# Kernel tuning notes

Hardware: AMD Instinct MI355X
Metric: run time of the kernel (lower is better)

Reference implementation:

```python
import jax, jax.numpy as jnp
import numpy as np

H = 51  # hidden size hard-coded in the module


def setup_inputs() -> dict:
    key = jax.random.key(0)
    ks = jax.random.split(key, 11)
    B, T = 1024, 512
    s = 1.0 / np.sqrt(H)
    u = lambda k, shape: jax.random.uniform(k, shape, jnp.float32, -s, s)
    return {
        "input": jax.random.normal(ks[0], (B, T), jnp.float32),
        "Wih1": u(ks[1], (4 * H, 1)),
        "Whh1": u(ks[2], (4 * H, H)),
        "bih1": u(ks[3], (4 * H,)),
        "bhh1": u(ks[4], (4 * H,)),
        "Wih2": u(ks[5], (4 * H, H)),
        "Whh2": u(ks[6], (4 * H, H)),
        "bih2": u(ks[7], (4 * H,)),
        "bhh2": u(ks[8], (4 * H,)),
        "Wl": u(ks[9], (1, H)),
        "bl": u(ks[10], (1,)),
        "future": 64,
    }


def _lstm_cell(x, h, c, Wih, Whh, b):
    # x: [B, in], h/c: [B, H]; PyTorch LSTMCell gate order: i, f, g, o
    g = x @ Wih.T + h @ Whh.T + b  # [B, 4H]
    i, f, gg, o = jnp.split(g, 4, axis=-1)
    c = jax.nn.sigmoid(f) * c + jax.nn.sigmoid(i) * jnp.tanh(gg)
    h = jax.nn.sigmoid(o) * jnp.tanh(c)
    return h, c


def reference(input, Wih1, Whh1, bih1, bhh1, Wih2, Whh2, bih2, bhh2, Wl, bl, future):
    B = input.shape[0]
    b1 = bih1 + bhh1
    b2 = bih2 + bhh2
    z = jnp.zeros((B, H), input.dtype)

    def step(carry, x_t):
        h1, c1, h2, c2 = carry
        h1, c1 = _lstm_cell(x_t[:, None], h1, c1, Wih1, Whh1, b1)
        h2, c2 = _lstm_cell(h1, h2, c2, Wih2, Whh2, b2)
        out = h2 @ Wl.T + bl  # [B, 1]
        return (h1, c1, h2, c2), out

    carry, outs = jax.lax.scan(step, (z, z, z, z), input.T)  # outs: [T, B, 1]

    if future > 0:
        def fstep(carry, _):
            h1, c1, h2, c2, out = carry
            h1, c1 = _lstm_cell(out, h1, c1, Wih1, Whh1, b1)
            h2, c2 = _lstm_cell(h1, h2, c2, Wih2, Whh2, b2)
            out = h2 @ Wl.T + bl
            return (h1, c1, h2, c2, out), out

        _, fouts = jax.lax.scan(fstep, (*carry, outs[-1]), None, length=future)
        outs = jnp.concatenate([outs, fouts], axis=0)  # [T+future, B, 1]

    return outs[..., 0].T  # [B, T+future]
```

## Files before the change

kernel.cpp:

```cpp
#include <hip/hip_runtime.h>
#include <stdint.h>

#define Hh    51
#define Bsz   1024
#define Tin   512
#define Ttot  576
#define NBB   8
#define BROWS 8
#define NW    7
#define BLK   (NW*64)
#define BST   136
#define WS    18

#define L2E   1.4426950408889634f
#define TL2E  2.8853900817779268f

typedef __attribute__((ext_vector_type(8))) _Float16 half8;
typedef __attribute__((ext_vector_type(4))) float f32x4;

__device__ __forceinline__ float rcpf(float x){ return __builtin_amdgcn_rcpf(x); }
__device__ __forceinline__ float exp2f_fast(float x){
#if __has_builtin(__builtin_amdgcn_exp2f)
    return __builtin_amdgcn_exp2f(x);
#else
    return exp2f(x);
#endif
}

__device__ __forceinline__ float cell_fuse(float vi, float vf, float vg,
                                           float vo, float& c){
    float Ei = exp2f_fast(-vi), Ef = exp2f_fast(-vf), Eg = exp2f_fast(-vg);
    float A = 1.f + Ef, B = 1.f + Ei, C = 1.f + Eg, D = 1.f - Eg;
    float BC = B*C;
    float R  = rcpf(A*BC);
    float cn = __builtin_fmaf(c, BC*R, (A*D)*R);
    c = cn;
    float Ec = exp2f_fast(fminf(-cn*TL2E, 120.f));
    float Eo = exp2f_fast(-vo);
    float R2 = rcpf((1.f+Eo)*(1.f+Ec));
    return (1.f - Ec) * R2;
}

__device__ __forceinline__ uint16_t f2h(float f){
    union{ _Float16 h; uint16_t u; } v; v.h = (_Float16)f;
    return v.u;
}

__device__ __forceinline__ float qsum(float x){
    x += __shfl_xor(x, 16, 64);
    x += __shfl_xor(x, 32, 64);
    return x;
}
#define MFMA __builtin_amdgcn_mfma_f32_16x16x32_f16

__global__ __launch_bounds__(BLK, 2)
void lstm_f16b(const float* __restrict__ inp,
               const float* __restrict__ Wih1,
               const float* __restrict__ Whh1,
               const float* __restrict__ bih1,
               const float* __restrict__ bhh1,
               const float* __restrict__ Wih2,
               const float* __restrict__ Whh2,
               const float* __restrict__ bih2,
               const float* __restrict__ bhh2,
               const float* __restrict__ Wl,
               const float* __restrict__ blp,
               float* __restrict__ outp)
{
    const int tid = threadIdx.x;
    const int wv  = tid >> 6, ln = tid & 63;
    const int quad = ln >> 4, nn = ln & 15;
    const bool lo = (nn < 8);
    const int ba  = nn & 7;
    const int b0  = blockIdx.x * NBB;

    __shared__ __align__(16) uint16_t Bh[2][BROWS*BST];
    __shared__ float wsum[2][NW*WS];

    for (int k = tid; k < BROWS*BST; k += BLK) { Bh[0][k] = 0; Bh[1][k] = 0; }
    if (tid < NW*WS) { wsum[0][tid] = 0.f; wsum[1][tid] = 0.f; }

    half8 a1[2][2], a2[2][4];
    f32x4 bias1[2], bias2[2], wih1v[2];
    float wlu[2];
#pragma unroll
    for (int tl = 0; tl < 2; ++tl) {
        const bool tv = (wv + 7*tl) < 13;
        const int lr = 16*(wv + 7*tl) + nn;
        const int ua_ = lr >> 2, ga = lr & 3;
        const bool av = tv && (ua_ < Hh);
        const int pr = av ? (ga*Hh + ua_) : 0;
        const float rs = (ga == 2) ? TL2E : L2E;
#pragma unroll
        for (int s = 0; s < 2; ++s)
#pragma unroll
            for (int j = 0; j < 8; ++j) {
                int k = 32*s + quad*8 + j;
                float w = (av && k < Hh) ? Whh1[pr*Hh + k]*rs : 0.f;
                a1[tl][s][j] = (_Float16)w;
            }
#pragma unroll
        for (int s = 0; s < 4; ++s)
#pragma unroll
            for (int j = 0; j < 8; ++j) {
                int k = 32*s + quad*8 + j;
                float w = 0.f;
                if (av) {
                    if (k < Hh)                    w = Wih2[pr*Hh + k]*rs;
                    else if (k >= 64 && k < 64+Hh) w = Whh2[pr*Hh + (k-64)]*rs;
                }
                a2[tl][s][j] = (_Float16)w;
            }
        const int u = 4*(wv + 7*tl) + quad;
        const bool uv = tv && (u < Hh);
#pragma unroll
        for (int i = 0; i < 4; ++i) {
            int pri = uv ? (i*Hh + u) : 0;
            float gs = (i == 2) ? TL2E : L2E;
            bias1[tl][i] = uv ? (bih1[pri] + bhh1[pri])*gs : 0.f;
            bias2[tl][i] = uv ? (bih2[pri] + bhh2[pri])*gs : 0.f;
            wih1v[tl][i] = uv ? Wih1[pri]*gs : 0.f;
        }
        wlu[tl] = uv ? Wl[u] : 0.f;
    }
    const float blv = blp[0];

    const int  ua  = 4*(wv + (lo ? 0 : 7)) + quad;
    const bool uva = (ua < Hh);
    const float wlua = lo ? wlu[0] : wlu[1];
    float c1 = 0.f, c2 = 0.f;

    {
        float b1a[4], w1a[4];
#pragma unroll
        for (int i = 0; i < 4; ++i) {
            b1a[i] = lo ? bias1[0][i] : bias1[1][i];
            w1a[i] = lo ? wih1v[0][i] : wih1v[1][i];
        }
        float x0 = inp[(size_t)(b0 + ba)*Tin];
        float vi = __builtin_fmaf(w1a[0], x0, b1a[0]);
        float vf = __builtin_fmaf(w1a[1], x0, b1a[1]);
        float vg = __builtin_fmaf(w1a[2], x0, b1a[2]);
        float vo = __builtin_fmaf(w1a[3], x0, b1a[3]);
        float h1n = cell_fuse(vi, vf, vg, vo, c1);
        if (uva) Bh[0][ba*BST + ua] = f2h(h1n);
    }
    float xreg = (Tin > 1) ? inp[(size_t)(b0 + ba)*Tin + 1] : 0.f;
    __syncthreads();

    for (int t = 0; t < Tin-1; ++t) {
        const int cur = t & 1, nxt = cur ^ 1;

        const uint16_t* rb = &Bh[cur][ba*BST + quad*8];
        half8 s0 = *(const half8*)(rb),      s1 = *(const half8*)(rb + 32);
        half8 s2 = *(const half8*)(rb + 64), s3 = *(const half8*)(rb + 96);

        if (wv == NW-1 && t > 0) {
            float osum = blv;
#pragma unroll
            for (int w = 0; w < NW; ++w)
                osum += wsum[nxt][w*WS + ba] + wsum[nxt][w*WS + 8 + ba];
            if (ln < NBB) outp[(size_t)(b0 + ln)*Ttot + (t-1)] = osum;
        }
        float xn = (t + 2 < Tin) ? inp[(size_t)(b0 + ba)*Tin + t + 2] : 0.f;

        f32x4 aA0 = bias2[0], aB0 = {0.f,0.f,0.f,0.f};
        f32x4 aA1 = bias2[1], aB1 = {0.f,0.f,0.f,0.f};
        f32x4 bA0, bA1, bB0 = {0.f,0.f,0.f,0.f}, bB1 = {0.f,0.f,0.f,0.f};
#pragma unroll
        for (int i = 0; i < 4; ++i) {
            bA0[i] = __builtin_fmaf(wih1v[0][i], xreg, bias1[0][i]);
            bA1[i] = __builtin_fmaf(wih1v[1][i], xreg, bias1[1][i]);
        }
        aA0 = MFMA(a2[0][0], s0, aA0, 0,0,0);  aB0 = MFMA(a2[0][1], s1, aB0, 0,0,0);
        aA1 = MFMA(a2[1][0], s0, aA1, 0,0,0);  aB1 = MFMA(a2[1][1], s1, aB1, 0,0,0);
        bA0 = MFMA(a1[0][0], s0, bA0, 0,0,0);  bB0 = MFMA(a1[0][1], s1, bB0, 0,0,0);
        bA1 = MFMA(a1[1][0], s0, bA1, 0,0,0);  bB1 = MFMA(a1[1][1], s1, bB1, 0,0,0);
        aA0 = MFMA(a2[0][2], s2, aA0, 0,0,0);  aB0 = MFMA(a2[0][3], s3, aB0, 0,0,0);
        aA1 = MFMA(a2[1][2], s2, aA1, 0,0,0);  aB1 = MFMA(a2[1][3], s3, aB1, 0,0,0);

        f32x4 g2t0 = aA0 + aB0, g2t1 = aA1 + aB1;
        f32x4 g1t0 = bA0 + bB0, g1t1 = bA1 + bB1;
        float g2[4], g1[4];
#pragma unroll
        for (int i = 0; i < 4; ++i) {
            g2[i] = lo ? g2t0[i] : g2t1[i];
            g1[i] = lo ? g1t0[i] : g1t1[i];
        }

        float h2v = cell_fuse(g2[0], g2[1], g2[2], g2[3], c2);
        float h1v = cell_fuse(g1[0], g1[1], g1[2], g1[3], c1);
        if (uva) {
            Bh[nxt][ba*BST + 64 + ua] = f2h(h2v);
            Bh[nxt][ba*BST      + ua] = f2h(h1v);
        }
        float part = qsum(wlua * h2v);
        if (ln < 16) wsum[cur][wv*WS + ln] = part;

        __syncthreads();
        xreg = xn;
    }

    for (int t = Tin-1; t < Ttot; ++t) {
        const int cur = t & 1, nxt = cur ^ 1;

        const uint16_t* rb = &Bh[cur][ba*BST + quad*8];
        half8 s0 = *(const half8*)(rb),      s1 = *(const half8*)(rb + 32);
        half8 s2 = *(const half8*)(rb + 64), s3 = *(const half8*)(rb + 96);

        if (wv == NW-1) {
            float osum = blv;
#pragma unroll
            for (int w = 0; w < NW; ++w)
                osum += wsum[nxt][w*WS + ba] + wsum[nxt][w*WS + 8 + ba];
            if (ln < NBB) outp[(size_t)(b0 + ln)*Ttot + (t-1)] = osum;
        }

        f32x4 aA0 = bias2[0], aB0 = {0.f,0.f,0.f,0.f};
        f32x4 aA1 = bias2[1], aB1 = {0.f,0.f,0.f,0.f};
        aA0 = MFMA(a2[0][0], s0, aA0, 0,0,0);  aB0 = MFMA(a2[0][1], s1, aB0, 0,0,0);
        aA1 = MFMA(a2[1][0], s0, aA1, 0,0,0);  aB1 = MFMA(a2[1][1], s1, aB1, 0,0,0);
        aA0 = MFMA(a2[0][2], s2, aA0, 0,0,0);  aB0 = MFMA(a2[0][3], s3, aB0, 0,0,0);
        aA1 = MFMA(a2[1][2], s2, aA1, 0,0,0);  aB1 = MFMA(a2[1][3], s3, aB1, 0,0,0);
        f32x4 g2t0 = aA0 + aB0, g2t1 = aA1 + aB1;
        float g2[4];
#pragma unroll
        for (int i = 0; i < 4; ++i) g2[i] = lo ? g2t0[i] : g2t1[i];
        float h2v = cell_fuse(g2[0], g2[1], g2[2], g2[3], c2);
        if (uva) Bh[nxt][ba*BST + 64 + ua] = f2h(h2v);
        float part = qsum(wlua * h2v);
        if (ln < 16) wsum[cur][wv*WS + ln] = part;
        __syncthreads();

        if (t + 1 < Ttot) {
            float osum = blv;
#pragma unroll
            for (int w = 0; w < NW; ++w)
                osum += wsum[cur][w*WS + ba] + wsum[cur][w*WS + 8 + ba];
            f32x4 bA0, bA1, bB0 = {0.f,0.f,0.f,0.f}, bB1 = {0.f,0.f,0.f,0.f};
#pragma unroll
            for (int i = 0; i < 4; ++i) {
                bA0[i] = __builtin_fmaf(wih1v[0][i], osum, bias1[0][i]);
                bA1[i] = __builtin_fmaf(wih1v[1][i], osum, bias1[1][i]);
            }
            bA0 = MFMA(a1[0][0], s0, bA0, 0,0,0);  bB0 = MFMA(a1[0][1], s1, bB0, 0,0,0);
            bA1 = MFMA(a1[1][0], s0, bA1, 0,0,0);  bB1 = MFMA(a1[1][1], s1, bB1, 0,0,0);
            f32x4 g1t0 = bA0 + bB0, g1t1 = bA1 + bB1;
            float g1[4];
#pragma unroll
            for (int i = 0; i < 4; ++i) g1[i] = lo ? g1t0[i] : g1t1[i];
            float h1v = cell_fuse(g1[0], g1[1], g1[2], g1[3], c1);
            if (uva) Bh[nxt][ba*BST + ua] = f2h(h1v);
            __syncthreads();
        }
    }

    if (wv == NW-1) {
        float osum = blv;
#pragma unroll
        for (int w = 0; w < NW; ++w)
            osum += wsum[(Ttot-1)&1][w*WS + ba] + wsum[(Ttot-1)&1][w*WS + 8 + ba];
        if (ln < NBB) outp[(size_t)(b0 + ln)*Ttot + (Ttot-1)] = osum;
    }
}

extern "C" void kernel_launch(void* const* d_in, const int* in_sizes, int n_in,
                              void* d_out, int out_size, void* d_ws, size_t ws_size,
                              hipStream_t stream) {
    (void)in_sizes; (void)n_in; (void)out_size; (void)d_ws; (void)ws_size;
    lstm_f16b<<<dim3(Bsz / NBB), dim3(BLK), 0, stream>>>(
        (const float*)d_in[0], (const float*)d_in[1],
        (const float*)d_in[2], (const float*)d_in[3],
        (const float*)d_in[4], (const float*)d_in[5],
        (const float*)d_in[6], (const float*)d_in[7],
        (const float*)d_in[8], (const float*)d_in[9],
        (const float*)d_in[10], (float*)d_out);
}
```

Baseline: 521.8 us.

## Split LSTM layers across separate wave groups within each block

Doubles the block to 14 waves: waves 0-6 compute only layer-2 gates and waves 7-13 compute only layer-1 gates, each holding only its own weight fragments. Per-wave MFMA and cell work in each step drops, shortening the serial critical path per timestep. In exchange the block becomes twice as large with one block per CU in the launch bounds, barrier cost grows with more waves, and occupancy and latency hiding change.

```diff
diff --git a/kernel.cpp b/kernel.cpp
--- a/kernel.cpp
+++ b/kernel.cpp
@@ -7,8 +7,9 @@
 #define Ttot  576
 #define NBB   8
 #define BROWS 8
-#define NW    7
-#define BLK   (NW*64)
+#define NTP   7
+#define NWV   14
+#define BLK   (NWV*64)
 #define BST   136
 #define WS    18
 
@@ -53,19 +54,19 @@
 }
 #define MFMA __builtin_amdgcn_mfma_f32_16x16x32_f16
 
-__global__ __launch_bounds__(BLK, 2)
-void lstm_f16b(const float* __restrict__ inp,
-               const float* __restrict__ Wih1,
-               const float* __restrict__ Whh1,
-               const float* __restrict__ bih1,
-               const float* __restrict__ bhh1,
-               const float* __restrict__ Wih2,
-               const float* __restrict__ Whh2,
-               const float* __restrict__ bih2,
-               const float* __restrict__ bhh2,
-               const float* __restrict__ Wl,
-               const float* __restrict__ blp,
-               float* __restrict__ outp)
+__global__ __launch_bounds__(BLK, 1)
+void lstm_f16s2(const float* __restrict__ inp,
+                const float* __restrict__ Wih1,
+                const float* __restrict__ Whh1,
+                const float* __restrict__ bih1,
+                const float* __restrict__ bhh1,
+                const float* __restrict__ Wih2,
+                const float* __restrict__ Whh2,
+                const float* __restrict__ bih2,
+                const float* __restrict__ bhh2,
+                const float* __restrict__ Wl,
+                const float* __restrict__ blp,
+                float* __restrict__ outp)
 {
     const int tid = threadIdx.x;
     const int wv  = tid >> 6, ln = tid & 63;
@@ -73,129 +74,138 @@
     const bool lo = (nn < 8);
     const int ba  = nn & 7;
     const int b0  = blockIdx.x * NBB;
+    const bool isL2 = (wv < NTP);
+    const int  wvv  = isL2 ? wv : wv - NTP;
 
     __shared__ __align__(16) uint16_t Bh[2][BROWS*BST];
-    __shared__ float wsum[2][NW*WS];
+    __shared__ float wsum[2][NTP*WS];
 
     for (int k = tid; k < BROWS*BST; k += BLK) { Bh[0][k] = 0; Bh[1][k] = 0; }
-    if (tid < NW*WS) { wsum[0][tid] = 0.f; wsum[1][tid] = 0.f; }
-
-    half8 a1[2][2], a2[2][4];
-    f32x4 bias1[2], bias2[2], wih1v[2];
+    if (tid < NTP*WS) { wsum[0][tid] = 0.f; wsum[1][tid] = 0.f; }
+
+    half8 af[8];
+    f32x4 bs[2], w1v[2];
     float wlu[2];
 #pragma unroll
     for (int tl = 0; tl < 2; ++tl) {
-        const bool tv = (wv + 7*tl) < 13;
-        const int lr = 16*(wv + 7*tl) + nn;
+        const bool tv = (wvv + 7*tl) < 13;
+        const int lr = 16*(wvv + 7*tl) + nn;
         const int ua_ = lr >> 2, ga = lr & 3;
         const bool av = tv && (ua_ < Hh);
         const int pr = av ? (ga*Hh + ua_) : 0;
         const float rs = (ga == 2) ? TL2E : L2E;
-#pragma unroll
-        for (int s = 0; s < 2; ++s)
-#pragma unroll
-            for (int j = 0; j < 8; ++j) {
-                int k = 32*s + quad*8 + j;
-                float w = (av && k < Hh) ? Whh1[pr*Hh + k]*rs : 0.f;
-                a1[tl][s][j] = (_Float16)w;
-            }
-#pragma unroll
-        for (int s = 0; s < 4; ++s)
-#pragma unroll
-            for (int j = 0; j < 8; ++j) {
-                int k = 32*s + quad*8 + j;
-                float w = 0.f;
-                if (av) {
-                    if (k < Hh)                    w = Wih2[pr*Hh + k]*rs;
-                    else if (k >= 64 && k < 64+Hh) w = Whh2[pr*Hh + (k-64)]*rs;
+        if (isL2) {
+#pragma unroll
+            for (int s = 0; s < 4; ++s)
+#pragma unroll
+                for (int j = 0; j < 8; ++j) {
+                    int k = 32*s + quad*8 + j;
+                    float w = 0.f;
+                    if (av) {
+                        if (k < Hh)                    w = Wih2[pr*Hh + k]*rs;
+                        else if (k >= 64 && k < 64+Hh) w = Whh2[pr*Hh + (k-64)]*rs;
+                    }
+                    af[tl*4+s][j] = (_Float16)w;
                 }
-                a2[tl][s][j] = (_Float16)w;
-            }
-        const int u = 4*(wv + 7*tl) + quad;
+        } else {
+#pragma unroll
+            for (int s = 0; s < 2; ++s)
+#pragma unroll
+                for (int j = 0; j < 8; ++j) {
+                    int k = 32*s + quad*8 + j;
+                    float w = (av && k < Hh) ? Whh1[pr*Hh + k]*rs : 0.f;
+                    af[tl*2+s][j] = (_Float16)w;
+                }
+        }
+        const int u = 4*(wvv + 7*tl) + quad;
         const bool uv = tv && (u < Hh);
 #pragma unroll
         for (int i = 0; i < 4; ++i) {
             int pri = uv ? (i*Hh + u) : 0;
             float gs = (i == 2) ? TL2E : L2E;
-            bias1[tl][i] = uv ? (bih1[pri] + bhh1[pri])*gs : 0.f;
-            bias2[tl][i] = uv ? (bih2[pri] + bhh2[pri])*gs : 0.f;
-            wih1v[tl][i] = uv ? Wih1[pri]*gs : 0.f;
-        }
-        wlu[tl] = uv ? Wl[u] : 0.f;
+            if (isL2) {
+                bs[tl][i]  = uv ? (bih2[pri] + bhh2[pri])*gs : 0.f;
+                w1v[tl][i] = 0.f;
+            } else {
+                bs[tl][i]  = uv ? (bih1[pri] + bhh1[pri])*gs : 0.f;
+                w1v[tl][i] = uv ? Wih1[pri]*gs : 0.f;
+            }
+        }
+        wlu[tl] = (isL2 && uv) ? Wl[u] : 0.f;
     }
     const float blv = blp[0];
 
-    const int  ua  = 4*(wv + (lo ? 0 : 7)) + quad;
+    const int  ua  = 4*(wvv + (lo ? 0 : 7)) + quad;
     const bool uva = (ua < Hh);
     const float wlua = lo ? wlu[0] : wlu[1];
-    float c1 = 0.f, c2 = 0.f;
-
-    {
+    float cst = 0.f;
+
+    if (!isL2) {
         float b1a[4], w1a[4];
 #pragma unroll
         for (int i = 0; i < 4; ++i) {
-            b1a[i] = lo ? bias1[0][i] : bias1[1][i];
-            w1a[i] = lo ? wih1v[0][i] : wih1v[1][i];
+            b1a[i] = lo ? bs[0][i] : bs[1][i];
+            w1a[i] = lo ? w1v[0][i] : w1v[1][i];
         }
         float x0 = inp[(size_t)(b0 + ba)*Tin];
         float vi = __builtin_fmaf(w1a[0], x0, b1a[0]);
         float vf = __builtin_fmaf(w1a[1], x0, b1a[1]);
         float vg = __builtin_fmaf(w1a[2], x0, b1a[2]);
         float vo = __builtin_fmaf(w1a[3], x0, b1a[3]);
-        float h1n = cell_fuse(vi, vf, vg, vo, c1);
+        float h1n = cell_fuse(vi, vf, vg, vo, cst);
         if (uva) Bh[0][ba*BST + ua] = f2h(h1n);
     }
-    float xreg = (Tin > 1) ? inp[(size_t)(b0 + ba)*Tin + 1] : 0.f;
+    float xreg = (!isL2 && Tin > 1) ? inp[(size_t)(b0 + ba)*Tin + 1] : 0.f;
     __syncthreads();
 
     for (int t = 0; t < Tin-1; ++t) {
         const int cur = t & 1, nxt = cur ^ 1;
 
         const uint16_t* rb = &Bh[cur][ba*BST + quad*8];
-        half8 s0 = *(const half8*)(rb),      s1 = *(const half8*)(rb + 32);
-        half8 s2 = *(const half8*)(rb + 64), s3 = *(const half8*)(rb + 96);
-
-        if (wv == NW-1 && t > 0) {
+        half8 s0 = *(const half8*)(rb), s1 = *(const half8*)(rb + 32);
+        half8 s2, s3;
+        if (isL2) { s2 = *(const half8*)(rb + 64); s3 = *(const half8*)(rb + 96); }
+
+        if (wv == NTP-1 && t > 0) {
             float osum = blv;
 #pragma unroll
-            for (int w = 0; w < NW; ++w)
+            for (int w = 0; w < NTP; ++w)
                 osum += wsum[nxt][w*WS + ba] + wsum[nxt][w*WS + 8 + ba];
             if (ln < NBB) outp[(size_t)(b0 + ln)*Ttot + (t-1)] = osum;
         }
-        float xn = (t + 2 < Tin) ? inp[(size_t)(b0 + ba)*Tin + t + 2] : 0.f;
-
-        f32x4 aA0 = bias2[0], aB0 = {0.f,0.f,0.f,0.f};
-        f32x4 aA1 = bias2[1], aB1 = {0.f,0.f,0.f,0.f};
-        f32x4 bA0, bA1, bB0 = {0.f,0.f,0.f,0.f}, bB1 = {0.f,0.f,0.f,0.f};
-#pragma unroll
-        for (int i = 0; i < 4; ++i) {
-            bA0[i] = __builtin_fmaf(wih1v[0][i], xreg, bias1[0][i]);
-            bA1[i] = __builtin_fmaf(wih1v[1][i], xreg, bias1[1][i]);
-        }
-        aA0 = MFMA(a2[0][0], s0, aA0, 0,0,0);  aB0 = MFMA(a2[0][1], s1, aB0, 0,0,0);
-        aA1 = MFMA(a2[1][0], s0, aA1, 0,0,0);  aB1 = MFMA(a2[1][1], s1, aB1, 0,0,0);
-        bA0 = MFMA(a1[0][0], s0, bA0, 0,0,0);  bB0 = MFMA(a1[0][1], s1, bB0, 0,0,0);
-        bA1 = MFMA(a1[1][0], s0, bA1, 0,0,0);  bB1 = MFMA(a1[1][1], s1, bB1, 0,0,0);
-        aA0 = MFMA(a2[0][2], s2, aA0, 0,0,0);  aB0 = MFMA(a2[0][3], s3, aB0, 0,0,0);
-        aA1 = MFMA(a2[1][2], s2, aA1, 0,0,0);  aB1 = MFMA(a2[1][3], s3, aB1, 0,0,0);
-
-        f32x4 g2t0 = aA0 + aB0, g2t1 = aA1 + aB1;
-        f32x4 g1t0 = bA0 + bB0, g1t1 = bA1 + bB1;
-        float g2[4], g1[4];
-#pragma unroll
-        for (int i = 0; i < 4; ++i) {
-            g2[i] = lo ? g2t0[i] : g2t1[i];
-            g1[i] = lo ? g1t0[i] : g1t1[i];
-        }
-
-        float h2v = cell_fuse(g2[0], g2[1], g2[2], g2[3], c2);
-        float h1v = cell_fuse(g1[0], g1[1], g1[2], g1[3], c1);
-        if (uva) {
-            Bh[nxt][ba*BST + 64 + ua] = f2h(h2v);
-            Bh[nxt][ba*BST      + ua] = f2h(h1v);
-        }
-        float part = qsum(wlua * h2v);
-        if (ln < 16) wsum[cur][wv*WS + ln] = part;
+        float xn = (!isL2 && t + 2 < Tin) ? inp[(size_t)(b0 + ba)*Tin + t + 2] : 0.f;
+
+        if (isL2) {
+            f32x4 aA0 = bs[0], aB0 = {0.f,0.f,0.f,0.f};
+            f32x4 aA1 = bs[1], aB1 = {0.f,0.f,0.f,0.f};
+            aA0 = MFMA(af[0], s0, aA0, 0,0,0);  aB0 = MFMA(af[1], s1, aB0, 0,0,0);
+            aA1 = MFMA(af[4], s0, aA1, 0,0,0);  aB1 = MFMA(af[5], s1, aB1, 0,0,0);
+            aA0 = MFMA(af[2], s2, aA0, 0,0,0);  aB0 = MFMA(af[3], s3, aB0, 0,0,0);
+            aA1 = MFMA(af[6], s2, aA1, 0,0,0);  aB1 = MFMA(af[7], s3, aB1, 0,0,0);
+            f32x4 gt0 = aA0 + aB0, gt1 = aA1 + aB1;
+            float g[4];
+#pragma unroll
+            for (int i = 0; i < 4; ++i) g[i] = lo ? gt0[i] : gt1[i];
+            float h2v = cell_fuse(g[0], g[1], g[2], g[3], cst);
+            if (uva) Bh[nxt][ba*BST + 64 + ua] = f2h(h2v);
+            float part = qsum(wlua * h2v);
+            if (ln < 16) wsum[cur][wvv*WS + ln] = part;
+        } else {
+            f32x4 bA0, bA1, bB0 = {0.f,0.f,0.f,0.f}, bB1 = {0.f,0.f,0.f,0.f};
+#pragma unroll
+            for (int i = 0; i < 4; ++i) {
+                bA0[i] = __builtin_fmaf(w1v[0][i], xreg, bs[0][i]);
+                bA1[i] = __builtin_fmaf(w1v[1][i], xreg, bs[1][i]);
+            }
+            bA0 = MFMA(af[0], s0, bA0, 0,0,0);  bB0 = MFMA(af[1], s1, bB0, 0,0,0);
+            bA1 = MFMA(af[2], s0, bA1, 0,0,0);  bB1 = MFMA(af[3], s1, bB1, 0,0,0);
+            f32x4 gt0 = bA0 + bB0, gt1 = bA1 + bB1;
+            float g[4];
+#pragma unroll
+            for (int i = 0; i < 4; ++i) g[i] = lo ? gt0[i] : gt1[i];
+            float h1v = cell_fuse(g[0], g[1], g[2], g[3], cst);
+            if (uva) Bh[nxt][ba*BST + ua] = f2h(h1v);
+        }
 
         __syncthreads();
         xreg = xn;
@@ -205,60 +215,65 @@
         const int cur = t & 1, nxt = cur ^ 1;
 
         const uint16_t* rb = &Bh[cur][ba*BST + quad*8];
-        half8 s0 = *(const half8*)(rb),      s1 = *(const half8*)(rb + 32);
-        half8 s2 = *(const half8*)(rb + 64), s3 = *(const half8*)(rb + 96);
-
-        if (wv == NW-1) {
+        half8 s0 = *(const half8*)(rb), s1 = *(const half8*)(rb + 32);
+        half8 s2, s3;
+        if (isL2) { s2 = *(const half8*)(rb + 64); s3 = *(const half8*)(rb + 96); }
+
+        if (wv == NTP-1) {
             float osum = blv;
 #pragma unroll
-            for (int w = 0; w < NW; ++w)
+            for (int w = 0; w < NTP; ++w)
                 osum += wsum[nxt][w*WS + ba] + wsum[nxt][w*WS + 8 + ba];
             if (ln < NBB) outp[(size_t)(b0 + ln)*Ttot + (t-1)] = osum;
         }
 
-        f32x4 aA0 = bias2[0], aB0 = {0.f,0.f,0.f,0.f};
-        f32x4 aA1 = bias2[1], aB1 = {0.f,0.f,0.f,0.f};
-        aA0 = MFMA(a2[0][0], s0, aA0, 0,0,0);  aB0 = MFMA(a2[0][1], s1, aB0, 0,0,0);
-        aA1 = MFMA(a2[1][0], s0, aA1, 0,0,0);  aB1 = MFMA(a2[1][1], s1, aB1, 0,0,0);
-        aA0 = MFMA(a2[0][2], s2, aA0, 0,0,0);  aB0 = MFMA(a2[0][3], s3, aB0, 0,0,0);
-        aA1 = MFMA(a2[1][2], s2, aA1, 0,0,0);  aB1 = MFMA(a2[1][3], s3, aB1, 0,0,0);
-        f32x4 g2t0 = aA0 + aB0, g2t1 = aA1 + aB1;
-        float g2[4];
-#pragma unroll
-        for (int i = 0; i < 4; ++i) g2[i] = lo ? g2t0[i] : g2t1[i];
-        float h2v = cell_fuse(g2[0], g2[1], g2[2], g2[3], c2);
-        if (uva) Bh[nxt][ba*BST + 64 + ua] = f2h(h2v);
-        float part = qsum(wlua * h2v);
-        if (ln < 16) wsum[cur][wv*WS + ln] = part;
+        if (isL2) {
+            f32x4 aA0 = bs[0], aB0 = {0.f,0.f,0.f,0.f};
+            f32x4 aA1 = bs[1], aB1 = {0.f,0.f,0.f,0.f};
+            aA0 = MFMA(af[0], s0, aA0, 0,0,0);  aB0 = MFMA(af[1], s1, aB0, 0,0,0);
+            aA1 = MFMA(af[4], s0, aA1, 0,0,0);  aB1 = MFMA(af[5], s1, aB1, 0,0,0);
+            aA0 = MFMA(af[2], s2, aA0, 0,0,0);  aB0 = MFMA(af[3], s3, aB0, 0,0,0);
+            aA1 = MFMA(af[6], s2, aA1, 0,0,0);  aB1 = MFMA(af[7], s3, aB1, 0,0,0);
+            f32x4 gt0 = aA0 + aB0, gt1 = aA1 + aB1;
+            float g[4];
+#pragma unroll
+            for (int i = 0; i < 4; ++i) g[i] = lo ? gt0[i] : gt1[i];
+            float h2v = cell_fuse(g[0], g[1], g[2], g[3], cst);
+            if (uva) Bh[nxt][ba*BST + 64 + ua] = f2h(h2v);
+            float part = qsum(wlua * h2v);
+            if (ln < 16) wsum[cur][wvv*WS + ln] = part;
+        }
         __syncthreads();
 
         if (t + 1 < Ttot) {
-            float osum = blv;
-#pragma unroll
-            for (int w = 0; w < NW; ++w)
-                osum += wsum[cur][w*WS + ba] + wsum[cur][w*WS + 8 + ba];
-            f32x4 bA0, bA1, bB0 = {0.f,0.f,0.f,0.f}, bB1 = {0.f,0.f,0.f,0.f};
-#pragma unroll
-            for (int i = 0; i < 4; ++i) {
-                bA0[i] = __builtin_fmaf(wih1v[0][i], osum, bias1[0][i]);
-                bA1[i] = __builtin_fmaf(wih1v[1][i], osum, bias1[1][i]);
+            if (!isL2) {
+                float osum = blv;
+#pragma unroll
+                for (int w = 0; w < NTP; ++w)
+                    osum += wsum[cur][w*WS + ba] + wsum[cur][w*WS + 8 + ba];
+                f32x4 bA0, bA1, bB0 = {0.f,0.f,0.f,0.f}, bB1 = {0.f,0.f,0.f,0.f};
+#pragma unroll
+                for (int i = 0; i < 4; ++i) {
+                    bA0[i] = __builtin_fmaf(w1v[0][i], osum, bs[0][i]);
+                    bA1[i] = __builtin_fmaf(w1v[1][i], osum, bs[1][i]);
+                }
+                bA0 = MFMA(af[0], s0, bA0, 0,0,0);  bB0 = MFMA(af[1], s1, bB0, 0,0,0);
+                bA1 = MFMA(af[2], s0, bA1, 0,0,0);  bB1 = MFMA(af[3], s1, bB1, 0,0,0);
+                f32x4 gt0 = bA0 + bB0, gt1 = bA1 + bB1;
+                float g[4];
+#pragma unroll
+                for (int i = 0; i < 4; ++i) g[i] = lo ? gt0[i] : gt1[i];
+                float h1v = cell_fuse(g[0], g[1], g[2], g[3], cst);
+                if (uva) Bh[nxt][ba*BST + ua] = f2h(h1v);
             }
-            bA0 = MFMA(a1[0][0], s0, bA0, 0,0,0);  bB0 = MFMA(a1[0][1], s1, bB0, 0,0,0);
-            bA1 = MFMA(a1[1][0], s0, bA1, 0,0,0);  bB1 = MFMA(a1[1][1], s1, bB1, 0,0,0);
-            f32x4 g1t0 = bA0 + bB0, g1t1 = bA1 + bB1;
-            float g1[4];
-#pragma unroll
-            for (int i = 0; i < 4; ++i) g1[i] = lo ? g1t0[i] : g1t1[i];
-            float h1v = cell_fuse(g1[0], g1[1], g1[2], g1[3], c1);
-            if (uva) Bh[nxt][ba*BST + ua] = f2h(h1v);
             __syncthreads();
         }
     }
 
-    if (wv == NW-1) {
+    if (wv == NTP-1) {
         float osum = blv;
 #pragma unroll
-        for (int w = 0; w < NW; ++w)
+        for (int w = 0; w < NTP; ++w)
             osum += wsum[(Ttot-1)&1][w*WS + ba] + wsum[(Ttot-1)&1][w*WS + 8 + ba];
         if (ln < NBB) outp[(size_t)(b0 + ln)*Ttot + (Ttot-1)] = osum;
     }
@@ -268,7 +283,7 @@
                               void* d_out, int out_size, void* d_ws, size_t ws_size,
                               hipStream_t stream) {
     (void)in_sizes; (void)n_in; (void)out_size; (void)d_ws; (void)ws_size;
-    lstm_f16b<<<dim3(Bsz / NBB), dim3(BLK), 0, stream>>>(
+    lstm_f16s2<<<dim3(Bsz / NBB), dim3(BLK), 0, stream>>>(
         (const float*)d_in[0], (const float*)d_in[1],
         (const float*)d_in[2], (const float*)d_in[3],
         (const float*)d_in[4], (const float*)d_in[5],
```

Result: faster. 496.4 us (-4.9%).
